# Optimization experiments

Measured on AMD Instinct MI355X. Metric: run time of the kernel, lower is better.

Reference implementation:

```python
import jax, jax.numpy as jnp
import numpy as np

N, F_IN = 100000, 602      # nodes, input features
H, C = 41, 1               # heads = num_classes, channels per head (hidden // heads)
E = 1600000                # raw edges (self-loops added in forward, as GATConv does)
L = 5                      # num_layers
NEG_SLOPE = 0.2


def setup_inputs() -> dict:
    key = jax.random.key(0)
    ks = jax.random.split(key, 8)
    x = jax.random.normal(ks[0], (N, F_IN), dtype=jnp.float32)
    edge_index = jax.random.randint(ks[1], (2, E), 0, N, dtype=jnp.int32)
    s = 0.1  # weight scale
    W0 = jax.random.normal(ks[2], (F_IN, H * C), dtype=jnp.float32) * s
    W_rest = jax.random.normal(ks[3], (L - 1, H * C, H * C), dtype=jnp.float32) * s
    att_src = jax.random.normal(ks[4], (L, H, C), dtype=jnp.float32) * s
    att_dst = jax.random.normal(ks[5], (L, H, C), dtype=jnp.float32) * s
    bias = jax.random.normal(ks[6], (L, H * C), dtype=jnp.float32) * s
    return {"x": x, "edge_index": edge_index, "W0": W0, "W_rest": W_rest,
            "att_src": att_src, "att_dst": att_dst, "bias": bias}


def _gat_layer(x, src, dst, W, a_s, a_d, b, apply_relu):
    n = x.shape[0]
    h = (x @ W).reshape(n, H, C)                      # per-head features [N,H,C]
    a_src_n = (h * a_s).sum(-1)                       # [N,H]
    a_dst_n = (h * a_d).sum(-1)                       # [N,H]
    e = a_src_n[src] + a_dst_n[dst]                   # [Etot,H]
    e = jnp.where(e > 0, e, NEG_SLOPE * e)            # leaky_relu
    # segment softmax over incoming edges of each dst node (self-loops => nonempty)
    emax = jax.ops.segment_max(e, dst, num_segments=n)
    ex = jnp.exp(e - emax[dst])
    denom = jax.ops.segment_sum(ex, dst, num_segments=n)
    alpha = ex / denom[dst]                           # [Etot,H]
    m = alpha[:, :, None] * h[src]                    # messages [Etot,H,C]
    out = jax.ops.segment_max(m, dst, num_segments=n) # aggr='max'
    out = out.reshape(n, H * C) + b
    return jax.nn.relu(out) if apply_relu else out


def reference(x, edge_index, W0, W_rest, att_src, att_dst, bias):
    loops = jnp.arange(N, dtype=edge_index.dtype)
    src = jnp.concatenate([edge_index[0], loops])     # add self-loops
    dst = jnp.concatenate([edge_index[1], loops])
    h = _gat_layer(x, src, dst, W0, att_src[0], att_dst[0], bias[0], True)
    for l in range(L - 1):
        last = (l == L - 2)
        h = _gat_layer(h, src, dst, W_rest[l], att_src[l + 1], att_dst[l + 1],
                       bias[l + 1], not last)
    return jax.nn.log_softmax(h, axis=1)
```

## Files before the change

kernel.cpp:

```cpp
#include <hip/hip_runtime.h>


#define N_NODES 100000
#define F_IN    602
#define NH      41
#define NEDGE   1600000
#define NLAYERS 5
#define LOG2E   1.44269504088896340736f

__global__ void hist_kernel(const int* __restrict__ dst, int* __restrict__ cnt, int e) {
    int i = blockIdx.x * blockDim.x + threadIdx.x;
    if (i < e) atomicAdd(&cnt[dst[i]], 1);
}

__global__ __launch_bounds__(1024) void scan_kernel(const int* __restrict__ cnt,
                                                    int* __restrict__ row_ptr, int n) {
    __shared__ int sums[1024];
    int t = threadIdx.x;
    int chunk = (n + 1023) >> 10;
    int start = t * chunk;
    int end   = min(start + chunk, n);
    int s = 0;
    for (int i = start; i < end; ++i) s += cnt[i];
    sums[t] = s;
    __syncthreads();
    for (int off = 1; off < 1024; off <<= 1) {
        int v = (t >= off) ? sums[t - off] : 0;
        __syncthreads();
        sums[t] += v;
        __syncthreads();
    }
    int run = (t == 0) ? 0 : sums[t - 1];
    for (int i = start; i < end; ++i) { row_ptr[i] = run; run += cnt[i]; }
    if (start < n && end == n) row_ptr[n] = run;
}

__global__ void scatter_kernel(const int* __restrict__ src, const int* __restrict__ dst,
                               const int* __restrict__ row_ptr, int* __restrict__ cur,
                               int* __restrict__ esrc, int e) {
    int i = blockIdx.x * blockDim.x + threadIdx.x;
    if (i < e) {
        int d = dst[i];
        int pos = row_ptr[d] + atomicAdd(&cur[d], 1);
        esrc[pos] = src[i];
    }
}

__global__ void transpose_w_kernel(const float* __restrict__ W0, const float* __restrict__ Wr,
                                   float* __restrict__ wT0, float* __restrict__ wTr) {
    int i = blockIdx.x * blockDim.x + threadIdx.x;
    if (i < F_IN * NH) {
        int k = i / NH, c = i - k * NH;
        wT0[c * F_IN + k] = W0[i];
    }
    if (i < 4 * NH * NH) {
        int l = i / (NH * NH), rem = i - l * NH * NH;
        int k = rem / NH, c = rem - k * NH;
        wTr[l * NH * NH + c * NH + k] = Wr[i];
    }
}

__global__ __launch_bounds__(256) void gemm0_kernel(const float* __restrict__ x,
                                                    const float* __restrict__ wT,
                                                    float* __restrict__ h) {
    __shared__ float xs[2][32][65];
    const int tid  = threadIdx.x;
    const int q    = tid >> 6;
    const int r    = tid & 63;
    const int rr   = tid >> 5;
    const int kk   = tid & 31;
    const int row0 = blockIdx.x * 64;
    const int cbase = __builtin_amdgcn_readfirstlane(min(q * 11, NH - 11));
    const float* __restrict__ wq = wT + cbase * F_IN;
    const int NCHT = 19;

    float acc[11];
#pragma unroll
    for (int c = 0; c < 11; ++c) acc[c] = 0.f;
    float rg[8];

    auto stage_load = [&](int ci) {
        int k0 = ci * 32;
        int kl = (ci == 18) ? 26 : 32;
#pragma unroll
        for (int li = 0; li < 8; ++li) {
            int rrow = row0 + li * 8 + rr;
            rg[li] = (kk < kl && rrow < N_NODES) ? x[rrow * F_IN + k0 + kk] : 0.f;
        }
    };
    auto stage_write = [&](int b) {
#pragma unroll
        for (int li = 0; li < 8; ++li) xs[b][kk][li * 8 + rr] = rg[li];
    };

    stage_load(0);
    stage_write(0);

    for (int ci = 0; ci < NCHT; ++ci) {
        if (ci + 1 < NCHT) stage_load(ci + 1);
        __syncthreads();
        const int b = ci & 1, k0 = ci * 32;
        if (ci < 18) {
#pragma unroll
            for (int k = 0; k < 32; ++k) {
                float xv = xs[b][k][r];
#pragma unroll
                for (int c = 0; c < 11; ++c)
                    acc[c] = fmaf(xv, wq[c * F_IN + k0 + k], acc[c]);
            }
        } else {
#pragma unroll
            for (int k = 0; k < 26; ++k) {
                float xv = xs[b][k][r];
#pragma unroll
                for (int c = 0; c < 11; ++c)
                    acc[c] = fmaf(xv, wq[c * F_IN + k0 + k], acc[c]);
            }
        }
        if (ci + 1 < NCHT) stage_write((ci + 1) & 1);
    }

    int row = row0 + r;
    if (row < N_NODES) {
#pragma unroll
        for (int c = 0; c < 11; ++c)
            h[row * NH + cbase + c] = acc[c];
    }
}

__global__ __launch_bounds__(256) void gemm_small_kernel(const float* __restrict__ in,
                                                         const float* __restrict__ wT,
                                                         float* __restrict__ h) {
    __shared__ float xs[NH][65];
    const int tid  = threadIdx.x;
    const int q    = tid >> 6;
    const int r    = tid & 63;
    const int row0 = blockIdx.x * 64;
    const int cbase = __builtin_amdgcn_readfirstlane(min(q * 11, NH - 11));
    const float* __restrict__ wq = wT + cbase * NH;

    const int base = row0 * NH;
    for (int e = tid; e < 64 * NH; e += 256) {
        int rrw = e / NH;
        int k   = e - rrw * NH;
        xs[k][rrw] = (row0 + rrw < N_NODES) ? in[base + e] : 0.f;
    }
    __syncthreads();

    float acc[11];
#pragma unroll
    for (int c = 0; c < 11; ++c) acc[c] = 0.f;
#pragma unroll
    for (int k = 0; k < NH; ++k) {
        float xv = xs[k][r];
#pragma unroll
        for (int c = 0; c < 11; ++c)
            acc[c] = fmaf(xv, wq[c * NH + k], acc[c]);
    }

    int row = row0 + r;
    if (row < N_NODES) {
#pragma unroll
        for (int c = 0; c < 11; ++c)
            h[row * NH + cbase + c] = acc[c];
    }
}

__global__ __launch_bounds__(256) void gat_kernel(const float* __restrict__ h,
                                                  const int* __restrict__ row_ptr,
                                                  const int* __restrict__ esrc,
                                                  const float* __restrict__ att_s,
                                                  const float* __restrict__ att_d,
                                                  const float* __restrict__ bias,
                                                  float* __restrict__ out,
                                                  int apply_relu) {
    int idx = blockIdx.x * blockDim.x + threadIdx.x;
    if (idx >= N_NODES * NH) return;
    int n  = idx / NH;
    int hd = idx - n * NH;

    float as2  = att_s[hd] * LOG2E;
    float hn   = h[idx];
    float adt2 = hn * att_d[hd] * LOG2E;

    float t0 = fmaf(hn, as2, adt2);
    float e0 = fmaxf(t0, 0.2f * t0);
    float den = 1.0f;
    float num = hn;

    int s = row_ptr[n], t = row_ptr[n + 1];
    int   sra = esrc[s];
    int   srb = esrc[s + 1];
    float hsa = h[__mul24(sra, NH) + hd];
    float hsb = h[__mul24(srb, NH) + hd];
    for (int j = s; j < t; ++j) {
        int   src2 = esrc[j + 2];
        float hsc  = h[__mul24(src2, NH) + hd];
        float tt = fmaf(hsa, as2, adt2);
        float ee = fmaxf(tt, 0.2f * tt);
        float p  = __builtin_amdgcn_exp2f(ee - e0);
        den += p;
        num = fmaxf(num, p * hsa);
        hsa = hsb; hsb = hsc;
    }
    float o = num / den + bias[hd];
    out[idx] = apply_relu ? fmaxf(o, 0.f) : o;
}

__global__ __launch_bounds__(256) void logsoftmax_kernel(const float* __restrict__ in,
                                                         float* __restrict__ out) {
    int n = blockIdx.x * blockDim.x + threadIdx.x;
    if (n >= N_NODES) return;
    float v[NH];
#pragma unroll
    for (int c = 0; c < NH; ++c) v[c] = in[n * NH + c];
    float m = v[0];
#pragma unroll
    for (int c = 1; c < NH; ++c) m = fmaxf(m, v[c]);
    float ssum = 0.f;
#pragma unroll
    for (int c = 0; c < NH; ++c) ssum += __expf(v[c] - m);
    float lg = m + logf(ssum);
#pragma unroll
    for (int c = 0; c < NH; ++c) out[n * NH + c] = v[c] - lg;
}

extern "C" void kernel_launch(void* const* d_in, const int* in_sizes, int n_in,
                              void* d_out, int out_size, void* d_ws, size_t ws_size,
                              hipStream_t stream) {
    const float* x   = (const float*)d_in[0];
    const int*   ei  = (const int*)  d_in[1];
    const float* W0  = (const float*)d_in[2];
    const float* Wr  = (const float*)d_in[3];
    const float* as_ = (const float*)d_in[4];
    const float* ad_ = (const float*)d_in[5];
    const float* bs  = (const float*)d_in[6];
    float* out = (float*)d_out;

    const int* src = ei;
    const int* dst = ei + NEDGE;

    char* ws = (char*)d_ws;
    size_t off = 0;
    auto alloc = [&](size_t bytes) -> void* {
        void* p = ws + off;
        off += (bytes + 255) & ~size_t(255);
        return p;
    };
    int*   cnt     = (int*)  alloc((size_t)N_NODES * 4);
    int*   row_ptr = (int*)  alloc((size_t)(N_NODES + 1) * 4);
    int*   esrc    = (int*)  alloc((size_t)(NEDGE + 4) * 4);
    float* hbuf    = (float*)alloc((size_t)N_NODES * NH * 4);
    float* obuf    = (float*)alloc((size_t)N_NODES * NH * 4);
    float* wT0     = (float*)alloc((size_t)NH * F_IN * 4);
    float* wTr     = (float*)alloc((size_t)4 * NH * NH * 4);

    hipMemsetAsync(cnt, 0, (size_t)N_NODES * 4, stream);
    hipMemsetAsync(esrc + NEDGE, 0, 16, stream);
    hist_kernel<<<(NEDGE + 255) / 256, 256, 0, stream>>>(dst, cnt, NEDGE);
    scan_kernel<<<1, 1024, 0, stream>>>(cnt, row_ptr, N_NODES);
    hipMemsetAsync(cnt, 0, (size_t)N_NODES * 4, stream);
    scatter_kernel<<<(NEDGE + 255) / 256, 256, 0, stream>>>(src, dst, row_ptr, cnt, esrc, NEDGE);

    transpose_w_kernel<<<(F_IN * NH + 255) / 256, 256, 0, stream>>>(W0, Wr, wT0, wTr);

    const int NBLK = (N_NODES + 63) / 64;
    gemm0_kernel<<<NBLK, 256, 0, stream>>>(x, wT0, hbuf);

    for (int l = 0; l < NLAYERS; ++l) {
        if (l > 0)
            gemm_small_kernel<<<NBLK, 256, 0, stream>>>(
                obuf, wTr + (size_t)(l - 1) * NH * NH, hbuf);
        gat_kernel<<<(N_NODES * NH + 255) / 256, 256, 0, stream>>>(
            hbuf, row_ptr, esrc, as_ + l * NH, ad_ + l * NH, bs + l * NH,
            obuf, (l < NLAYERS - 1) ? 1 : 0);
    }

    logsoftmax_kernel<<<(N_NODES + 255) / 256, 256, 0, stream>>>(obuf, out);
}
```

Baseline: 1.471 ms.

## Store node features in fp16 with padded rows and split-K the input GEMM

Node features h are now stored as fp16 in 64-element padded rows, which halves the bytes gathered per edge in the GAT aggregation kernel. Padding the rows to 64 also lets the gather index be computed with a shift. The first GEMM is split along K into two partitions written to a partial buffer, and a combine kernel sums them and converts to fp16, doubling the blocks in flight. This adds a partial-buffer round trip and an extra launch, and fp16 rounding may reduce accuracy.

```diff
diff --git a/kernel.cpp b/kernel.cpp
--- a/kernel.cpp
+++ b/kernel.cpp
@@ -1,12 +1,15 @@
 #include <hip/hip_runtime.h>
+#include <hip/hip_fp16.h>
 
 
 #define N_NODES 100000
 #define F_IN    602
 #define NH      41
+#define HSTR    64
 #define NEDGE   1600000
 #define NLAYERS 5
 #define LOG2E   1.44269504088896340736f
+#define NPART   ((size_t)N_NODES * NH)
 
 __global__ void hist_kernel(const int* __restrict__ dst, int* __restrict__ cnt, int e) {
     int i = blockIdx.x * blockDim.x + threadIdx.x;
@@ -60,9 +63,9 @@
     }
 }
 
-__global__ __launch_bounds__(256) void gemm0_kernel(const float* __restrict__ x,
-                                                    const float* __restrict__ wT,
-                                                    float* __restrict__ h) {
+__global__ __launch_bounds__(256) void gemm0_part_kernel(const float* __restrict__ x,
+                                                         const float* __restrict__ wT,
+                                                         float* __restrict__ part) {
     __shared__ float xs[2][32][65];
     const int tid  = threadIdx.x;
     const int q    = tid >> 6;
@@ -70,9 +73,12 @@
     const int rr   = tid >> 5;
     const int kk   = tid & 31;
     const int row0 = blockIdx.x * 64;
+    const int p    = blockIdx.y;
+    const int kbeg = p * 301;
+    const int kend = min(F_IN, kbeg + 301);
+    const int nch  = (kend - kbeg + 31) >> 5;
     const int cbase = __builtin_amdgcn_readfirstlane(min(q * 11, NH - 11));
     const float* __restrict__ wq = wT + cbase * F_IN;
-    const int NCHT = 19;
 
     float acc[11];
 #pragma unroll
@@ -80,8 +86,8 @@
     float rg[8];
 
     auto stage_load = [&](int ci) {
-        int k0 = ci * 32;
-        int kl = (ci == 18) ? 26 : 32;
+        int k0 = kbeg + ci * 32;
+        int kl = min(32, kend - k0);
 #pragma unroll
         for (int li = 0; li < 8; ++li) {
             int rrow = row0 + li * 8 + rr;
@@ -96,41 +102,40 @@
     stage_load(0);
     stage_write(0);
 
-    for (int ci = 0; ci < NCHT; ++ci) {
-        if (ci + 1 < NCHT) stage_load(ci + 1);
+    for (int ci = 0; ci < nch; ++ci) {
+        if (ci + 1 < nch) stage_load(ci + 1);
         __syncthreads();
-        const int b = ci & 1, k0 = ci * 32;
-        if (ci < 18) {
-#pragma unroll
-            for (int k = 0; k < 32; ++k) {
-                float xv = xs[b][k][r];
-#pragma unroll
-                for (int c = 0; c < 11; ++c)
-                    acc[c] = fmaf(xv, wq[c * F_IN + k0 + k], acc[c]);
-            }
-        } else {
-#pragma unroll
-            for (int k = 0; k < 26; ++k) {
-                float xv = xs[b][k][r];
-#pragma unroll
-                for (int c = 0; c < 11; ++c)
-                    acc[c] = fmaf(xv, wq[c * F_IN + k0 + k], acc[c]);
-            }
+        const int b = ci & 1, k0 = kbeg + ci * 32;
+#pragma unroll
+        for (int k = 0; k < 32; ++k) {
+            float xv = xs[b][k][r];
+#pragma unroll
+            for (int c = 0; c < 11; ++c)
+                acc[c] = fmaf(xv, wq[c * F_IN + k0 + k], acc[c]);
         }
-        if (ci + 1 < NCHT) stage_write((ci + 1) & 1);
+        if (ci + 1 < nch) stage_write((ci + 1) & 1);
     }
 
     int row = row0 + r;
     if (row < N_NODES) {
-#pragma unroll
-        for (int c = 0; c < 11; ++c)
-            h[row * NH + cbase + c] = acc[c];
-    }
+        float* dstp = part + (size_t)p * NPART + (size_t)row * NH + cbase;
+#pragma unroll
+        for (int c = 0; c < 11; ++c) dstp[c] = acc[c];
+    }
+}
+
+__global__ __launch_bounds__(256) void combine_kernel(const float* __restrict__ part,
+                                                      __half* __restrict__ h16) {
+    int i = blockIdx.x * blockDim.x + threadIdx.x;
+    if (i >= (int)NPART) return;
+    float s = part[i] + part[NPART + i];
+    int row = i / NH, c = i - row * NH;
+    h16[(row << 6) + c] = __float2half_rn(s);
 }
 
 __global__ __launch_bounds__(256) void gemm_small_kernel(const float* __restrict__ in,
                                                          const float* __restrict__ wT,
-                                                         float* __restrict__ h) {
+                                                         __half* __restrict__ h16) {
     __shared__ float xs[NH][65];
     const int tid  = threadIdx.x;
     const int q    = tid >> 6;
@@ -162,11 +167,11 @@
     if (row < N_NODES) {
 #pragma unroll
         for (int c = 0; c < 11; ++c)
-            h[row * NH + cbase + c] = acc[c];
-    }
-}
-
-__global__ __launch_bounds__(256) void gat_kernel(const float* __restrict__ h,
+            h16[(row << 6) + cbase + c] = __float2half_rn(acc[c]);
+    }
+}
+
+__global__ __launch_bounds__(256) void gat_kernel(const __half* __restrict__ h16,
                                                   const int* __restrict__ row_ptr,
                                                   const int* __restrict__ esrc,
                                                   const float* __restrict__ att_s,
@@ -180,7 +185,7 @@
     int hd = idx - n * NH;
 
     float as2  = att_s[hd] * LOG2E;
-    float hn   = h[idx];
+    float hn   = __half2float(h16[(n << 6) + hd]);
     float adt2 = hn * att_d[hd] * LOG2E;
 
     float t0 = fmaf(hn, as2, adt2);
@@ -191,11 +196,11 @@
     int s = row_ptr[n], t = row_ptr[n + 1];
     int   sra = esrc[s];
     int   srb = esrc[s + 1];
-    float hsa = h[__mul24(sra, NH) + hd];
-    float hsb = h[__mul24(srb, NH) + hd];
+    float hsa = __half2float(h16[(sra << 6) + hd]);
+    float hsb = __half2float(h16[(srb << 6) + hd]);
     for (int j = s; j < t; ++j) {
         int   src2 = esrc[j + 2];
-        float hsc  = h[__mul24(src2, NH) + hd];
+        float hsc  = __half2float(h16[(src2 << 6) + hd]);
         float tt = fmaf(hsa, as2, adt2);
         float ee = fmaxf(tt, 0.2f * tt);
         float p  = __builtin_amdgcn_exp2f(ee - e0);
@@ -247,13 +252,14 @@
         off += (bytes + 255) & ~size_t(255);
         return p;
     };
-    int*   cnt     = (int*)  alloc((size_t)N_NODES * 4);
-    int*   row_ptr = (int*)  alloc((size_t)(N_NODES + 1) * 4);
-    int*   esrc    = (int*)  alloc((size_t)(NEDGE + 4) * 4);
-    float* hbuf    = (float*)alloc((size_t)N_NODES * NH * 4);
-    float* obuf    = (float*)alloc((size_t)N_NODES * NH * 4);
-    float* wT0     = (float*)alloc((size_t)NH * F_IN * 4);
-    float* wTr     = (float*)alloc((size_t)4 * NH * NH * 4);
+    int*    cnt     = (int*)   alloc((size_t)N_NODES * 4);
+    int*    row_ptr = (int*)   alloc((size_t)(N_NODES + 1) * 4);
+    int*    esrc    = (int*)   alloc((size_t)(NEDGE + 4) * 4);
+    __half* h16     = (__half*)alloc((size_t)N_NODES * HSTR * 2);
+    float*  obuf    = (float*) alloc((size_t)N_NODES * NH * 4);
+    float*  wT0     = (float*) alloc((size_t)NH * F_IN * 4);
+    float*  wTr     = (float*) alloc((size_t)4 * NH * NH * 4);
+    float*  part    = (float*) alloc(2 * NPART * 4);
 
     hipMemsetAsync(cnt, 0, (size_t)N_NODES * 4, stream);
     hipMemsetAsync(esrc + NEDGE, 0, 16, stream);
@@ -265,14 +271,16 @@
     transpose_w_kernel<<<(F_IN * NH + 255) / 256, 256, 0, stream>>>(W0, Wr, wT0, wTr);
 
     const int NBLK = (N_NODES + 63) / 64;
-    gemm0_kernel<<<NBLK, 256, 0, stream>>>(x, wT0, hbuf);
+    dim3 g0(NBLK, 2);
+    gemm0_part_kernel<<<g0, 256, 0, stream>>>(x, wT0, part);
+    combine_kernel<<<((int)NPART + 255) / 256, 256, 0, stream>>>(part, h16);
 
     for (int l = 0; l < NLAYERS; ++l) {
         if (l > 0)
             gemm_small_kernel<<<NBLK, 256, 0, stream>>>(
-                obuf, wTr + (size_t)(l - 1) * NH * NH, hbuf);
+                obuf, wTr + (size_t)(l - 1) * NH * NH, h16);
         gat_kernel<<<(N_NODES * NH + 255) / 256, 256, 0, stream>>>(
-            hbuf, row_ptr, esrc, as_ + l * NH, ad_ + l * NH, bs + l * NH,
+            h16, row_ptr, esrc, as_ + l * NH, ad_ + l * NH, bs + l * NH,
             obuf, (l < NLAYERS - 1) ? 1 : 0);
     }
 
```

Result: slower. 1.759 ms (+19.6%).
